# Kernel optimization log

Measured on AMD Instinct MI355X. Metric: run time of the kernel, lower is better.

The kernel has to match this reference:

```python
import jax, jax.numpy as jnp
import numpy as np

B, S, D, E, L = 8, 512, 768, 768, 4000

def setup_inputs() -> dict:
    key = jax.random.key(0)
    k1, k2, k3, k4 = jax.random.split(key, 4)
    last_hidden_state = jax.random.normal(k1, (B, S, D), dtype=jnp.float32)
    label_feat = jax.random.normal(k2, (L, E), dtype=jnp.float32)
    # nn.Linear(D, E): weight [E, D], bias [E]; xavier-ish scale
    W = jax.random.normal(k3, (E, D), dtype=jnp.float32) * (1.0 / np.sqrt(D))
    bias = jax.random.normal(k4, (E,), dtype=jnp.float32) * 0.01
    return {"last_hidden_state": last_hidden_state, "label_feat": label_feat, "W": W, "bias": bias}

def reference(last_hidden_state, label_feat, W, bias):
    # proj: tanh(Linear(last_hidden_state))  -> [B, S, E]
    proj = jnp.tanh(jnp.einsum('bsd,ed->bse', last_hidden_state, W) + bias)
    # scores: bmm(label_feat [B,L,E], proj^T [B,E,S]) -> [B, L, S]
    scores = jnp.einsum('le,bse->bls', label_feat, proj)
    # softmax over dim=1 (the LABEL dim), as in the original
    weights = jax.nn.softmax(scores, axis=1)
    # attn: bmm(weights [B,L,S], last_hidden_state [B,S,D]) -> [B, L, D]
    attn_output = jnp.einsum('bls,bsd->bld', weights, last_hidden_state)
    return (weights, attn_output)
```

## Files before the change

### kernel.cpp

```cpp
#include <hip/hip_runtime.h>
#include <hip/hip_bf16.h>
#include <cmath>

typedef __attribute__((ext_vector_type(8))) short short8;
typedef __attribute__((ext_vector_type(4))) float f32x4;

#define SM_CH 16
#define WCH   32

__device__ inline ushort f2bf(float x) {
    union { float f; unsigned u; } v; v.f = x;
    unsigned r = v.u + 0x7FFF + ((v.u >> 16) & 1);
    return (ushort)(r >> 16);
}

__device__ inline void split2(float x, ushort& hi, ushort& lo) {
    union { float f; unsigned u; } v; v.f = x;
    hi = (ushort)(v.u >> 16);
    union { float f; unsigned u; } h; h.u = v.u & 0xFFFF0000u;
    union { float f; unsigned u; } d; d.f = x - h.f;
    lo = (ushort)(d.u >> 16);
}

__device__ inline int swz(int row, int byte_in_row) {
    return row * 128 + (byte_in_row ^ ((row & 7) << 4));
}

__device__ inline void gload16(const void* g, void* lds) {
    __builtin_amdgcn_global_load_lds(
        (const __attribute__((address_space(1))) unsigned int*)g,
        (__attribute__((address_space(3))) unsigned int*)lds, 16, 0, 0);
}

__device__ inline void xcd_remap(int& bx, int& by, int& bz) {
    unsigned nx = gridDim.x, ny = gridDim.y;
    unsigned nwg = nx * ny * gridDim.z;
    unsigned id = blockIdx.x + nx * (blockIdx.y + ny * blockIdx.z);
    unsigned q = nwg >> 3;
    unsigned s = (id & 7) * q + (id >> 3);
    bx = s % nx; unsigned r = s / nx;
    by = r % ny; bz = r / ny;
}

template<int ROWS, int KS>
__device__ inline void stage_plane(const ushort* __restrict__ src,
                                   char* plane, int t, int rbase, int rmax)
{
    #pragma unroll
    for (int s = 0; s < ROWS / 64; ++s) {
        const int row = s * 64 + (t >> 3);
        const int col = (((t & 7) * 16) ^ ((row & 7) << 4)) >> 1;
        const int gr  = min(rbase + row, rmax);
        gload16(src + (long long)gr * KS + col,
                plane + s * 8192 + (t >> 6) * 1024);
    }
}

template<bool SPLIT3, int BM, int MREP, bool STATS, int NT, int KS, int VMN>
__global__ __launch_bounds__(512, 2) void mfma8(
    const ushort* __restrict__ AH, const ushort* __restrict__ AL,
    const ushort* __restrict__ BH, const ushort* __restrict__ BL,
    float* __restrict__ Cb, float* __restrict__ pmo, float* __restrict__ pso,
    int M, int N, long long sA, long long sB, long long sC)
{
    extern __shared__ char smem[];
    constexpr int ABYTES = BM * 128;

    int bx, by, bz; xcd_remap(bx, by, bz);
    const int bm = bx * BM;
    const int bn = by * 256;
    const long long z = bz;

    const ushort* AHb = AH + z * sA;
    const ushort* ALb = SPLIT3 ? (AL + z * sA) : AHb;
    const ushort* BHb = BH + z * sB;
    const ushort* BLb = SPLIT3 ? (BL + z * sB) : BHb;

    const int t    = threadIdx.x;
    const int lane = t & 63;
    const int w    = t >> 6;
    const int wr   = w >> 2;
    const int wc   = w & 3;
    const int lrow = lane & 15;
    const int kg16 = (lane >> 4) * 16;

    const ushort* Ap; const ushort* Bp; int kc;
#define SELPLANES(tt_)                                                        \
    do {                                                                      \
        if constexpr (SPLIT3) {                                               \
            Ap = ((tt_) < 24) ? AHb : ALb;                                    \
            Bp = (((tt_) < 12) || ((tt_) >= 24)) ? BHb : BLb;                 \
            int seg_ = ((tt_) < 12) ? (tt_) : (((tt_) < 24) ? (tt_) - 12      \
                                                            : (tt_) - 24);   \
            kc = seg_ * 64;                                                   \
        } else { Ap = AHb; Bp = BHb; kc = (tt_) * 64; }                       \
    } while (0)

    SELPLANES(0);
    stage_plane<BM, KS>(Ap + kc, smem, t, bm, M - 1);
    stage_plane<256, KS>(Bp + kc, smem + 2 * ABYTES, t, bn, N - 1);
    SELPLANES(1);
    stage_plane<BM, KS>(Ap + kc, smem + ABYTES, t, bm, M - 1);
    stage_plane<256, KS>(Bp + kc, smem + 2 * ABYTES + 32768, t, bn, N - 1);
    if constexpr (VMN == 8) asm volatile("s_waitcnt vmcnt(8)" ::: "memory");
    else                    asm volatile("s_waitcnt vmcnt(6)" ::: "memory");
    __builtin_amdgcn_s_barrier();

    f32x4 acc[MREP][4] = {};

    for (int tt = 0; tt < NT; ++tt) {
        const int cur = tt & 1;
        char* Ab = smem + cur * ABYTES;
        char* Bb = smem + 2 * ABYTES + cur * 32768;

        __builtin_amdgcn_s_setprio(1);
        short8 bf[4][2];
        #pragma unroll
        for (int n = 0; n < 4; ++n)
            #pragma unroll
            for (int ks = 0; ks < 2; ++ks)
                bf[n][ks] = *(const short8*)(Bb + swz(wc * 64 + n * 16 + lrow,
                                                      ks * 64 + kg16));
        #pragma unroll
        for (int q = 0; q < MREP / 2; ++q) {
            short8 af[2][2];
            #pragma unroll
            for (int mi = 0; mi < 2; ++mi)
                #pragma unroll
                for (int ks = 0; ks < 2; ++ks)
                    af[mi][ks] = *(const short8*)(Ab +
                        swz(wr * (BM / 2) + (q * 2 + mi) * 16 + lrow,
                            ks * 64 + kg16));
            #pragma unroll
            for (int ks = 0; ks < 2; ++ks)
                #pragma unroll
                for (int mi = 0; mi < 2; ++mi)
                    #pragma unroll
                    for (int n = 0; n < 4; ++n)
                        acc[q * 2 + mi][n] = __builtin_amdgcn_mfma_f32_16x16x32_bf16(
                            af[mi][ks], bf[n][ks], acc[q * 2 + mi][n], 0, 0, 0);
        }
        __builtin_amdgcn_s_setprio(0);

        asm volatile("s_waitcnt lgkmcnt(0)" ::: "memory");
        __builtin_amdgcn_s_barrier();

        if (tt + 2 < NT) {
            SELPLANES(tt + 2);
            stage_plane<BM, KS>(Ap + kc, smem + cur * ABYTES, t, bm, M - 1);
            stage_plane<256, KS>(Bp + kc, smem + 2 * ABYTES + cur * 32768,
                                 t, bn, N - 1);
            if constexpr (VMN == 8)
                asm volatile("s_waitcnt vmcnt(8)" ::: "memory");
            else
                asm volatile("s_waitcnt vmcnt(6)" ::: "memory");
        } else {
            asm volatile("s_waitcnt vmcnt(0)" ::: "memory");
        }
        __builtin_amdgcn_s_barrier();
    }
#undef SELPLANES

    float* C = Cb + z * sC;
    const int r0 = bm + wr * (BM / 2) + (lane >> 4) * 4;
    const int c0 = bn + wc * 64 + (lane & 15);
    #pragma unroll
    for (int n = 0; n < 4; ++n) {
        const int col = c0 + n * 16;
        #pragma unroll
        for (int mi = 0; mi < MREP; ++mi) {
            #pragma unroll
            for (int r = 0; r < 4; ++r) {
                const int row = r0 + mi * 16 + r;
                if (row < M) C[(long long)row * N + col] = acc[mi][n][r];
            }
        }
    }

    if constexpr (STATS) {
        __syncthreads();
        float* red = (float*)smem;
        const int slot = wr * 4 + (lane >> 4);
        const int colb = wc * 64 + (lane & 15);

        float lm[4];
        #pragma unroll
        for (int n = 0; n < 4; ++n) {
            float v = -INFINITY;
            #pragma unroll
            for (int mi = 0; mi < MREP; ++mi)
                #pragma unroll
                for (int r = 0; r < 4; ++r)
                    if (r0 + mi * 16 + r < M) v = fmaxf(v, acc[mi][n][r]);
            lm[n] = v;
        }
        #pragma unroll
        for (int n = 0; n < 4; ++n)
            red[(colb + n * 16) * 8 + slot] = lm[n];
        __syncthreads();
        float cm[4];
        #pragma unroll
        for (int n = 0; n < 4; ++n) {
            float v = -INFINITY;
            #pragma unroll
            for (int s8 = 0; s8 < 8; ++s8)
                v = fmaxf(v, red[(colb + n * 16) * 8 + s8]);
            cm[n] = v;
        }
        __syncthreads();
        float ls[4];
        #pragma unroll
        for (int n = 0; n < 4; ++n) {
            float sum = 0.f;
            #pragma unroll
            for (int mi = 0; mi < MREP; ++mi)
                #pragma unroll
                for (int r = 0; r < 4; ++r)
                    if (r0 + mi * 16 + r < M) sum += __expf(acc[mi][n][r] - cm[n]);
            ls[n] = sum;
        }
        #pragma unroll
        for (int n = 0; n < 4; ++n)
            red[(colb + n * 16) * 8 + slot] = ls[n];
        __syncthreads();
        if (slot == 0) {
            #pragma unroll
            for (int n = 0; n < 4; ++n) {
                float sum = 0.f;
                #pragma unroll
                for (int s8 = 0; s8 < 8; ++s8)
                    sum += red[(colb + n * 16) * 8 + s8];
                const int col = bn + colb + n * 16;
                pmo[(z * SM_CH + bx) * N + col] = cm[n];
                pso[(z * SM_CH + bx) * N + col] = sum;
            }
        }
    }
}

__global__ __launch_bounds__(256) void split_planes_kernel(
    const float* __restrict__ in, ushort* __restrict__ H,
    ushort* __restrict__ L, long long n4)
{
    long long i = (long long)blockIdx.x * 256 + threadIdx.x;
    if (i >= n4) return;
    float4 v = *(const float4*)(in + i * 4);
    ushort h[4], l[4];
    split2(v.x, h[0], l[0]); split2(v.y, h[1], l[1]);
    split2(v.z, h[2], l[2]); split2(v.w, h[3], l[3]);
    *(ushort4*)(H + i * 4) = *(ushort4*)h;
    *(ushort4*)(L + i * 4) = *(ushort4*)l;
}

__global__ __launch_bounds__(256) void mfma_proj(
    const float* __restrict__ Ab, const float* __restrict__ Bb,
    ushort* __restrict__ CH, ushort* __restrict__ CL,
    const float* __restrict__ bias, int M, int N, int K)
{
    extern __shared__ char smem[];
    char* Ah = smem;
    char* Al = smem + 16384;
    char* Bh = smem + 32768;
    char* Bl = smem + 49152;

    int bx, by, bz; xcd_remap(bx, by, bz);
    const int bm = bx * 128;
    const int bn = by * 128;

    const int t  = threadIdx.x;
    const int srow = t >> 1;
    const int skh  = (t & 1) * 32;
    const float* ap = Ab + (long long)min(bm + srow, M - 1) * K + skh;
    const float* bp = Bb + (long long)min(bn + srow, N - 1) * K + skh;

    const int lane = t & 63;
    const int w    = t >> 6;
    const int wm   = (w >> 1) * 64;
    const int wn   = (w & 1) * 64;
    const int lrow = lane & 15;
    const int kg16 = (lane >> 4) * 16;

    f32x4 acc[4][4] = {};

    for (int k0 = 0; k0 < K; k0 += 64) {
        #pragma unroll
        for (int j = 0; j < 4; ++j) {
            float xs[8];
            *(float4*)&xs[0] = *(const float4*)(ap + k0 + j * 8);
            *(float4*)&xs[4] = *(const float4*)(ap + k0 + j * 8 + 4);
            ushort oh[8], ol[8];
            #pragma unroll
            for (int i = 0; i < 8; ++i) split2(xs[i], oh[i], ol[i]);
            const int off = swz(srow, skh * 2 + j * 16);
            *(uint4*)(Ah + off) = *(uint4*)oh;
            *(uint4*)(Al + off) = *(uint4*)ol;
        }
        #pragma unroll
        for (int j = 0; j < 4; ++j) {
            float xs[8];
            *(float4*)&xs[0] = *(const float4*)(bp + k0 + j * 8);
            *(float4*)&xs[4] = *(const float4*)(bp + k0 + j * 8 + 4);
            ushort oh[8], ol[8];
            #pragma unroll
            for (int i = 0; i < 8; ++i) split2(xs[i], oh[i], ol[i]);
            const int off = swz(srow, skh * 2 + j * 16);
            *(uint4*)(Bh + off) = *(uint4*)oh;
            *(uint4*)(Bl + off) = *(uint4*)ol;
        }
        __syncthreads();

        #pragma unroll
        for (int kk = 0; kk < 2; ++kk) {
            short8 ah[4], al[4];
            #pragma unroll
            for (int mi = 0; mi < 4; ++mi) {
                const int off = swz(wm + mi * 16 + lrow, kk * 64 + kg16);
                ah[mi] = *(const short8*)(Ah + off);
                al[mi] = *(const short8*)(Al + off);
            }
            #pragma unroll
            for (int ni = 0; ni < 4; ++ni) {
                const int off = swz(wn + ni * 16 + lrow, kk * 64 + kg16);
                short8 bh = *(const short8*)(Bh + off);
                short8 bl = *(const short8*)(Bl + off);
                #pragma unroll
                for (int mi = 0; mi < 4; ++mi) {
                    acc[mi][ni] = __builtin_amdgcn_mfma_f32_16x16x32_bf16(al[mi], bh, acc[mi][ni], 0, 0, 0);
                    acc[mi][ni] = __builtin_amdgcn_mfma_f32_16x16x32_bf16(ah[mi], bl, acc[mi][ni], 0, 0, 0);
                    acc[mi][ni] = __builtin_amdgcn_mfma_f32_16x16x32_bf16(ah[mi], bh, acc[mi][ni], 0, 0, 0);
                }
            }
        }
        __syncthreads();
    }

    const int r0 = bm + wm + (lane >> 4) * 4;
    const int c0 = bn + wn + (lane & 15);
    #pragma unroll
    for (int ni = 0; ni < 4; ++ni) {
        const int col = c0 + ni * 16;
        const float bv = bias[col];
        #pragma unroll
        for (int mi = 0; mi < 4; ++mi) {
            #pragma unroll
            for (int r = 0; r < 4; ++r) {
                const int row = r0 + mi * 16 + r;
                if (row < M) {
                    float x = tanhf(acc[mi][ni][r] + bv);
                    ushort h, l;
                    split2(x, h, l);
                    CH[(long long)row * N + col] = h;
                    CL[(long long)row * N + col] = l;
                }
            }
        }
    }
}

__global__ __launch_bounds__(256) void transpose_bf16_kernel(
    const float* __restrict__ in, ushort* __restrict__ out, int S, int D)
{
    __shared__ float tile[32][33];
    const int b = blockIdx.z;
    const int s0 = blockIdx.x * 32, d0 = blockIdx.y * 32;
    const int tx = threadIdx.x & 31, ty = threadIdx.x >> 5;
    const float* ip = in + (long long)b * S * D;
    #pragma unroll
    for (int i = 0; i < 32; i += 8)
        tile[ty + i][tx] = ip[(long long)(s0 + ty + i) * D + d0 + tx];
    __syncthreads();
    ushort* op = out + (long long)b * S * D;
    #pragma unroll
    for (int i = 0; i < 32; i += 8)
        op[(long long)(d0 + ty + i) * S + s0 + tx] = f2bf(tile[tx][ty + i]);
}

__global__ __launch_bounds__(256) void softmax_merge_kernel(
    const float* __restrict__ pm, const float* __restrict__ ps,
    float* __restrict__ fm, float* __restrict__ fsinv, int S)
{
    int s = blockIdx.x * 256 + threadIdx.x;
    int b = blockIdx.y;
    float m = -INFINITY;
    #pragma unroll
    for (int c = 0; c < SM_CH; ++c)
        m = fmaxf(m, pm[(b * SM_CH + c) * S + s]);
    float sum = 0.f;
    #pragma unroll
    for (int c = 0; c < SM_CH; ++c)
        sum += ps[(b * SM_CH + c) * S + s] * __expf(pm[(b * SM_CH + c) * S + s] - m);
    fm[b * S + s] = m;
    fsinv[b * S + s] = 1.f / sum;
}

__global__ __launch_bounds__(256) void softmax_write_kernel(
    float* __restrict__ scores, const float* __restrict__ fm,
    const float* __restrict__ fsinv, int L, int S, int chlen,
    ushort* __restrict__ wbf)
{
    int s = blockIdx.x * 256 + threadIdx.x;
    int c = blockIdx.y;
    int b = blockIdx.z;
    float m   = fm[b * S + s];
    float inv = fsinv[b * S + s];
    float* p = scores + (long long)b * L * S + s;
    ushort* q = wbf + (long long)b * L * S + s;
    int l0 = c * chlen;
    int l1 = min(L, l0 + chlen);
    for (int l = l0; l < l1; ++l) {
        float x = p[(long long)l * S];
        float v = __expf(x - m) * inv;
        p[(long long)l * S] = v;
        q[(long long)l * S] = f2bf(v);
    }
}

extern "C" void kernel_launch(void* const* d_in, const int* in_sizes, int n_in,
                              void* d_out, int out_size, void* d_ws, size_t ws_size,
                              hipStream_t stream)
{
    const int Bn = 8, S = 512, D = 768, E = 768, L = 4000;
    const float* lhs   = (const float*)d_in[0];
    const float* label = (const float*)d_in[1];
    const float* W     = (const float*)d_in[2];
    const float* bias  = (const float*)d_in[3];

    float* weights = (float*)d_out;
    float* attn    = (float*)d_out + (long long)Bn * L * S;

    const long long nLE  = (long long)L * E;
    const long long nBSE = (long long)Bn * S * E;
    const long long nBDS = (long long)Bn * D * S;
    const long long nBLS = (long long)Bn * L * S;

    ushort* labelH = (ushort*)d_ws;
    ushort* labelL = labelH + nLE;
    ushort* projH  = labelL + nLE;
    ushort* projL  = projH + nBSE;
    ushort* lhsT   = projL + nBSE;
    ushort* wbf    = lhsT + nBDS;
    float*  pm     = (float*)(wbf + nBLS);
    float*  ps     = pm + Bn * SM_CH * S;
    float*  fm     = ps + Bn * SM_CH * S;
    float*  fsinv  = fm + Bn * S;

    auto scoresK = mfma8<true, 256, 8, true, 36, 768, 8>;
    auto attnK   = mfma8<false, 128, 4, false, 8, 512, 6>;
    hipFuncSetAttribute((const void*)scoresK,
                        hipFuncAttributeMaxDynamicSharedMemorySize, 131072);
    hipFuncSetAttribute((const void*)attnK,
                        hipFuncAttributeMaxDynamicSharedMemorySize, 98304);

    transpose_bf16_kernel<<<dim3(S / 32, D / 32, Bn), 256, 0, stream>>>(
        lhs, lhsT, S, D);
    split_planes_kernel<<<(int)(nLE / 4 + 255) / 256, 256, 0, stream>>>(
        label, labelH, labelL, nLE / 4);

    mfma_proj<<<dim3((Bn * S) / 128, E / 128, 1), 256, 65536, stream>>>(
        lhs, W, projH, projL, bias, Bn * S, E, D);

    scoresK<<<dim3((L + 255) / 256, S / 256, Bn), 512, 131072, stream>>>(
        labelH, labelL, projH, projL, weights, pm, ps,
        L, S, 0LL, (long long)S * E, (long long)L * S);

    softmax_merge_kernel<<<dim3(S / 256, Bn), 256, 0, stream>>>(
        pm, ps, fm, fsinv, S);
    softmax_write_kernel<<<dim3(S / 256, WCH, Bn), 256, 0, stream>>>(
        weights, fm, fsinv, L, S, (L + WCH - 1) / WCH, wbf);

    attnK<<<dim3((L + 127) / 128, D / 256, Bn), 512, 98304, stream>>>(
        wbf, nullptr, lhsT, nullptr, attn, nullptr, nullptr,
        L, D, (long long)L * S, (long long)D * S, (long long)L * D);
}
```

Measured before the change: 250.8 us.

## Stage hi/lo bf16 planes together in scores GEMM and fold softmax merge into write

The split-bf16 scores GEMM now loads the hi and lo halves of each 32-wide K chunk into one LDS tile and issues all three cross products (lo·hi, hi·lo, hi·hi) from one set of fragment reads. This replaces three separate 12-step K passes over different plane pairs with 24 steps. The aim is to read each A and B plane once instead of re-reading the hi planes, and to raise MFMA density per LDS load. Separately, the softmax merge kernel is removed and its max/sum reduction is recomputed in every softmax-write block. That saves one launch but repeats the small merge work across the 32 chunks.

New measurement: 243.9 us, median of 3. 2.7% less time.

```diff
diff --git a/kernel.cpp b/kernel.cpp
--- a/kernel.cpp
+++ b/kernel.cpp
@@ -42,39 +42,22 @@
     by = r % ny; bz = r / ny;
 }
 
-template<int ROWS, int KS>
-__device__ inline void stage_plane(const ushort* __restrict__ src,
-                                   char* plane, int t, int rbase, int rmax)
-{
-    #pragma unroll
-    for (int s = 0; s < ROWS / 64; ++s) {
-        const int row = s * 64 + (t >> 3);
-        const int col = (((t & 7) * 16) ^ ((row & 7) << 4)) >> 1;
-        const int gr  = min(rbase + row, rmax);
-        gload16(src + (long long)gr * KS + col,
-                plane + s * 8192 + (t >> 6) * 1024);
-    }
-}
-
-template<bool SPLIT3, int BM, int MREP, bool STATS, int NT, int KS, int VMN>
-__global__ __launch_bounds__(512, 2) void mfma8(
+__global__ __launch_bounds__(512, 2) void mfma_sc2(
     const ushort* __restrict__ AH, const ushort* __restrict__ AL,
     const ushort* __restrict__ BH, const ushort* __restrict__ BL,
     float* __restrict__ Cb, float* __restrict__ pmo, float* __restrict__ pso,
-    int M, int N, long long sA, long long sB, long long sC)
+    int M, int N, long long sB, long long sC)
 {
     extern __shared__ char smem[];
-    constexpr int ABYTES = BM * 128;
+    const int K = 768;
 
     int bx, by, bz; xcd_remap(bx, by, bz);
-    const int bm = bx * BM;
+    const int bm = bx * 256;
     const int bn = by * 256;
     const long long z = bz;
 
-    const ushort* AHb = AH + z * sA;
-    const ushort* ALb = SPLIT3 ? (AL + z * sA) : AHb;
     const ushort* BHb = BH + z * sB;
-    const ushort* BLb = SPLIT3 ? (BL + z * sB) : BHb;
+    const ushort* BLb = BL + z * sB;
 
     const int t    = threadIdx.x;
     const int lane = t & 63;
@@ -84,29 +67,203 @@
     const int lrow = lane & 15;
     const int kg16 = (lane >> 4) * 16;
 
-    const ushort* Ap; const ushort* Bp; int kc;
-#define SELPLANES(tt_)                                                        \
-    do {                                                                      \
-        if constexpr (SPLIT3) {                                               \
-            Ap = ((tt_) < 24) ? AHb : ALb;                                    \
-            Bp = (((tt_) < 12) || ((tt_) >= 24)) ? BHb : BLb;                 \
-            int seg_ = ((tt_) < 12) ? (tt_) : (((tt_) < 24) ? (tt_) - 12      \
-                                                            : (tt_) - 24);   \
-            kc = seg_ * 64;                                                   \
-        } else { Ap = AHb; Bp = BHb; kc = (tt_) * 64; }                       \
-    } while (0)
-
-    SELPLANES(0);
-    stage_plane<BM, KS>(Ap + kc, smem, t, bm, M - 1);
-    stage_plane<256, KS>(Bp + kc, smem + 2 * ABYTES, t, bn, N - 1);
-    SELPLANES(1);
-    stage_plane<BM, KS>(Ap + kc, smem + ABYTES, t, bm, M - 1);
-    stage_plane<256, KS>(Bp + kc, smem + 2 * ABYTES + 32768, t, bn, N - 1);
-    if constexpr (VMN == 8) asm volatile("s_waitcnt vmcnt(8)" ::: "memory");
-    else                    asm volatile("s_waitcnt vmcnt(6)" ::: "memory");
+    const ushort* srcA[4]; const ushort* srcB[4]; int ldsO[4];
+    #pragma unroll
+    for (int i = 0; i < 4; ++i) {
+        const int row  = w * 32 + i * 8 + (lane >> 3);
+        const int q    = (lane & 7) ^ (row & 7);
+        const int colo = (q & 3) * 8;
+        srcA[i] = ((q < 4) ? AH : AL) + (long long)min(bm + row, M - 1) * K + colo;
+        srcB[i] = ((q < 4) ? BHb : BLb) + (long long)(bn + row) * K + colo;
+        ldsO[i] = w * 4096 + i * 1024;
+    }
+
+#define STAGE(k0_, cur_)                                                      \
+    {                                                                         \
+        _Pragma("unroll")                                                     \
+        for (int i = 0; i < 4; ++i) {                                         \
+            gload16(srcA[i] + (k0_), smem + (cur_) * 32768 + ldsO[i]);        \
+            gload16(srcB[i] + (k0_), smem + 65536 + (cur_) * 32768 + ldsO[i]);\
+        }                                                                     \
+    }
+
+    STAGE(0, 0);
+    STAGE(32, 1);
+    asm volatile("s_waitcnt vmcnt(8)" ::: "memory");
     __builtin_amdgcn_s_barrier();
 
-    f32x4 acc[MREP][4] = {};
+    f32x4 acc[8][4] = {};
+
+    for (int tt = 0; tt < 24; ++tt) {
+        const int cur = tt & 1;
+        const char* Ab = smem + cur * 32768;
+        const char* Bb = smem + 65536 + cur * 32768;
+
+        __builtin_amdgcn_s_setprio(1);
+        short8 bh[4], bl[4];
+        #pragma unroll
+        for (int n = 0; n < 4; ++n) {
+            bh[n] = *(const short8*)(Bb + swz(wc * 64 + n * 16 + lrow, kg16));
+            bl[n] = *(const short8*)(Bb + swz(wc * 64 + n * 16 + lrow, 64 + kg16));
+        }
+        #pragma unroll
+        for (int g = 0; g < 2; ++g) {
+            short8 ah[4], al[4];
+            #pragma unroll
+            for (int m4 = 0; m4 < 4; ++m4) {
+                const int r = wr * 128 + (g * 4 + m4) * 16 + lrow;
+                ah[m4] = *(const short8*)(Ab + swz(r, kg16));
+                al[m4] = *(const short8*)(Ab + swz(r, 64 + kg16));
+            }
+            #pragma unroll
+            for (int m4 = 0; m4 < 4; ++m4)
+                #pragma unroll
+                for (int n = 0; n < 4; ++n) {
+                    acc[g*4+m4][n] = __builtin_amdgcn_mfma_f32_16x16x32_bf16(
+                        al[m4], bh[n], acc[g*4+m4][n], 0, 0, 0);
+                    acc[g*4+m4][n] = __builtin_amdgcn_mfma_f32_16x16x32_bf16(
+                        ah[m4], bl[n], acc[g*4+m4][n], 0, 0, 0);
+                    acc[g*4+m4][n] = __builtin_amdgcn_mfma_f32_16x16x32_bf16(
+                        ah[m4], bh[n], acc[g*4+m4][n], 0, 0, 0);
+                }
+        }
+        __builtin_amdgcn_s_setprio(0);
+
+        asm volatile("s_waitcnt lgkmcnt(0)" ::: "memory");
+        __builtin_amdgcn_s_barrier();
+
+        if (tt + 2 < 24) {
+            STAGE((tt + 2) * 32, cur);
+            asm volatile("s_waitcnt vmcnt(8)" ::: "memory");
+        } else {
+            asm volatile("s_waitcnt vmcnt(0)" ::: "memory");
+        }
+        __builtin_amdgcn_s_barrier();
+    }
+#undef STAGE
+
+    float* C = Cb + z * sC;
+    const int r0 = bm + wr * 128 + (lane >> 4) * 4;
+    const int c0 = bn + wc * 64 + (lane & 15);
+    #pragma unroll
+    for (int n = 0; n < 4; ++n) {
+        const int col = c0 + n * 16;
+        #pragma unroll
+        for (int mi = 0; mi < 8; ++mi) {
+            #pragma unroll
+            for (int r = 0; r < 4; ++r) {
+                const int row = r0 + mi * 16 + r;
+                if (row < M) C[(long long)row * N + col] = acc[mi][n][r];
+            }
+        }
+    }
+
+    __syncthreads();
+    float* red = (float*)smem;
+    const int slot = wr * 4 + (lane >> 4);
+    const int colb = wc * 64 + (lane & 15);
+
+    float lm[4];
+    #pragma unroll
+    for (int n = 0; n < 4; ++n) {
+        float v = -INFINITY;
+        #pragma unroll
+        for (int mi = 0; mi < 8; ++mi)
+            #pragma unroll
+            for (int r = 0; r < 4; ++r)
+                if (r0 + mi * 16 + r < M) v = fmaxf(v, acc[mi][n][r]);
+        lm[n] = v;
+    }
+    #pragma unroll
+    for (int n = 0; n < 4; ++n)
+        red[(colb + n * 16) * 8 + slot] = lm[n];
+    __syncthreads();
+    float cm[4];
+    #pragma unroll
+    for (int n = 0; n < 4; ++n) {
+        float v = -INFINITY;
+        #pragma unroll
+        for (int s8 = 0; s8 < 8; ++s8)
+            v = fmaxf(v, red[(colb + n * 16) * 8 + s8]);
+        cm[n] = v;
+    }
+    __syncthreads();
+    float ls[4];
+    #pragma unroll
+    for (int n = 0; n < 4; ++n) {
+        float sum = 0.f;
+        #pragma unroll
+        for (int mi = 0; mi < 8; ++mi)
+            #pragma unroll
+            for (int r = 0; r < 4; ++r)
+                if (r0 + mi * 16 + r < M) sum += __expf(acc[mi][n][r] - cm[n]);
+        ls[n] = sum;
+    }
+    #pragma unroll
+    for (int n = 0; n < 4; ++n)
+        red[(colb + n * 16) * 8 + slot] = ls[n];
+    __syncthreads();
+    if (slot == 0) {
+        #pragma unroll
+        for (int n = 0; n < 4; ++n) {
+            float sum = 0.f;
+            #pragma unroll
+            for (int s8 = 0; s8 < 8; ++s8)
+                sum += red[(colb + n * 16) * 8 + s8];
+            const int col = bn + colb + n * 16;
+            pmo[(z * SM_CH + bx) * N + col] = cm[n];
+            pso[(z * SM_CH + bx) * N + col] = sum;
+        }
+    }
+}
+
+template<int ROWS, int KS>
+__device__ inline void stage_plane(const ushort* __restrict__ src,
+                                   char* plane, int t, int rbase, int rmax)
+{
+    #pragma unroll
+    for (int s = 0; s < ROWS / 64; ++s) {
+        const int row = s * 64 + (t >> 3);
+        const int col = (((t & 7) * 16) ^ ((row & 7) << 4)) >> 1;
+        const int gr  = min(rbase + row, rmax);
+        gload16(src + (long long)gr * KS + col,
+                plane + s * 8192 + (t >> 6) * 1024);
+    }
+}
+
+__global__ __launch_bounds__(512, 2) void mfma_attn8(
+    const ushort* __restrict__ A, const ushort* __restrict__ B,
+    float* __restrict__ Cb, int M, int N,
+    long long sA, long long sB, long long sC)
+{
+    extern __shared__ char smem[];
+    constexpr int ABYTES = 128 * 128;
+    constexpr int NT = 8, KS = 512;
+
+    int bx, by, bz; xcd_remap(bx, by, bz);
+    const int bm = bx * 128;
+    const int bn = by * 256;
+    const long long z = bz;
+
+    const ushort* Ab_g = A + z * sA;
+    const ushort* Bb_g = B + z * sB;
+
+    const int t    = threadIdx.x;
+    const int lane = t & 63;
+    const int w    = t >> 6;
+    const int wr   = w >> 2;
+    const int wc   = w & 3;
+    const int lrow = lane & 15;
+    const int kg16 = (lane >> 4) * 16;
+
+    stage_plane<128, KS>(Ab_g, smem, t, bm, M - 1);
+    stage_plane<256, KS>(Bb_g, smem + 2 * ABYTES, t, bn, N - 1);
+    stage_plane<128, KS>(Ab_g + 64, smem + ABYTES, t, bm, M - 1);
+    stage_plane<256, KS>(Bb_g + 64, smem + 2 * ABYTES + 32768, t, bn, N - 1);
+    asm volatile("s_waitcnt vmcnt(6)" ::: "memory");
+    __builtin_amdgcn_s_barrier();
+
+    f32x4 acc[4][4] = {};
 
     for (int tt = 0; tt < NT; ++tt) {
         const int cur = tt & 1;
@@ -122,15 +279,14 @@
                 bf[n][ks] = *(const short8*)(Bb + swz(wc * 64 + n * 16 + lrow,
                                                       ks * 64 + kg16));
         #pragma unroll
-        for (int q = 0; q < MREP / 2; ++q) {
+        for (int q = 0; q < 2; ++q) {
             short8 af[2][2];
             #pragma unroll
             for (int mi = 0; mi < 2; ++mi)
                 #pragma unroll
                 for (int ks = 0; ks < 2; ++ks)
                     af[mi][ks] = *(const short8*)(Ab +
-                        swz(wr * (BM / 2) + (q * 2 + mi) * 16 + lrow,
-                            ks * 64 + kg16));
+                        swz(wr * 64 + (q * 2 + mi) * 16 + lrow, ks * 64 + kg16));
             #pragma unroll
             for (int ks = 0; ks < 2; ++ks)
                 #pragma unroll
@@ -146,93 +302,29 @@
         __builtin_amdgcn_s_barrier();
 
         if (tt + 2 < NT) {
-            SELPLANES(tt + 2);
-            stage_plane<BM, KS>(Ap + kc, smem + cur * ABYTES, t, bm, M - 1);
-            stage_plane<256, KS>(Bp + kc, smem + 2 * ABYTES + cur * 32768,
-                                 t, bn, N - 1);
-            if constexpr (VMN == 8)
-                asm volatile("s_waitcnt vmcnt(8)" ::: "memory");
-            else
-                asm volatile("s_waitcnt vmcnt(6)" ::: "memory");
+            stage_plane<128, KS>(Ab_g + (tt + 2) * 64, smem + cur * ABYTES,
+                                 t, bm, M - 1);
+            stage_plane<256, KS>(Bb_g + (tt + 2) * 64,
+                                 smem + 2 * ABYTES + cur * 32768, t, bn, N - 1);
+            asm volatile("s_waitcnt vmcnt(6)" ::: "memory");
         } else {
             asm volatile("s_waitcnt vmcnt(0)" ::: "memory");
         }
         __builtin_amdgcn_s_barrier();
     }
-#undef SELPLANES
 
     float* C = Cb + z * sC;
-    const int r0 = bm + wr * (BM / 2) + (lane >> 4) * 4;
+    const int r0 = bm + wr * 64 + (lane >> 4) * 4;
     const int c0 = bn + wc * 64 + (lane & 15);
     #pragma unroll
     for (int n = 0; n < 4; ++n) {
         const int col = c0 + n * 16;
         #pragma unroll
-        for (int mi = 0; mi < MREP; ++mi) {
+        for (int mi = 0; mi < 4; ++mi) {
             #pragma unroll
             for (int r = 0; r < 4; ++r) {
                 const int row = r0 + mi * 16 + r;
                 if (row < M) C[(long long)row * N + col] = acc[mi][n][r];
-            }
-        }
-    }
-
-    if constexpr (STATS) {
-        __syncthreads();
-        float* red = (float*)smem;
-        const int slot = wr * 4 + (lane >> 4);
-        const int colb = wc * 64 + (lane & 15);
-
-        float lm[4];
-        #pragma unroll
-        for (int n = 0; n < 4; ++n) {
-            float v = -INFINITY;
-            #pragma unroll
-            for (int mi = 0; mi < MREP; ++mi)
-                #pragma unroll
-                for (int r = 0; r < 4; ++r)
-                    if (r0 + mi * 16 + r < M) v = fmaxf(v, acc[mi][n][r]);
-            lm[n] = v;
-        }
-        #pragma unroll
-        for (int n = 0; n < 4; ++n)
-            red[(colb + n * 16) * 8 + slot] = lm[n];
-        __syncthreads();
-        float cm[4];
-        #pragma unroll
-        for (int n = 0; n < 4; ++n) {
-            float v = -INFINITY;
-            #pragma unroll
-            for (int s8 = 0; s8 < 8; ++s8)
-                v = fmaxf(v, red[(colb + n * 16) * 8 + s8]);
-            cm[n] = v;
-        }
-        __syncthreads();
-        float ls[4];
-        #pragma unroll
-        for (int n = 0; n < 4; ++n) {
-            float sum = 0.f;
-            #pragma unroll
-            for (int mi = 0; mi < MREP; ++mi)
-                #pragma unroll
-                for (int r = 0; r < 4; ++r)
-                    if (r0 + mi * 16 + r < M) sum += __expf(acc[mi][n][r] - cm[n]);
-            ls[n] = sum;
-        }
-        #pragma unroll
-        for (int n = 0; n < 4; ++n)
-            red[(colb + n * 16) * 8 + slot] = ls[n];
-        __syncthreads();
-        if (slot == 0) {
-            #pragma unroll
-            for (int n = 0; n < 4; ++n) {
-                float sum = 0.f;
-                #pragma unroll
-                for (int s8 = 0; s8 < 8; ++s8)
-                    sum += red[(colb + n * 16) * 8 + s8];
-                const int col = bn + colb + n * 16;
-                pmo[(z * SM_CH + bx) * N + col] = cm[n];
-                pso[(z * SM_CH + bx) * N + col] = sum;
             }
         }
     }
@@ -375,34 +467,25 @@
         op[(long long)(d0 + ty + i) * S + s0 + tx] = f2bf(tile[tx][ty + i]);
 }
 
-__global__ __launch_bounds__(256) void softmax_merge_kernel(
-    const float* __restrict__ pm, const float* __restrict__ ps,
-    float* __restrict__ fm, float* __restrict__ fsinv, int S)
-{
-    int s = blockIdx.x * 256 + threadIdx.x;
-    int b = blockIdx.y;
-    float m = -INFINITY;
-    #pragma unroll
-    for (int c = 0; c < SM_CH; ++c)
-        m = fmaxf(m, pm[(b * SM_CH + c) * S + s]);
-    float sum = 0.f;
-    #pragma unroll
-    for (int c = 0; c < SM_CH; ++c)
-        sum += ps[(b * SM_CH + c) * S + s] * __expf(pm[(b * SM_CH + c) * S + s] - m);
-    fm[b * S + s] = m;
-    fsinv[b * S + s] = 1.f / sum;
-}
-
-__global__ __launch_bounds__(256) void softmax_write_kernel(
-    float* __restrict__ scores, const float* __restrict__ fm,
-    const float* __restrict__ fsinv, int L, int S, int chlen,
+__global__ __launch_bounds__(256) void softmax_write2_kernel(
+    float* __restrict__ scores, const float* __restrict__ pm,
+    const float* __restrict__ ps, int L, int S, int chlen,
     ushort* __restrict__ wbf)
 {
     int s = blockIdx.x * 256 + threadIdx.x;
     int c = blockIdx.y;
     int b = blockIdx.z;
-    float m   = fm[b * S + s];
-    float inv = fsinv[b * S + s];
+
+    float m = -INFINITY;
+    #pragma unroll
+    for (int k = 0; k < SM_CH; ++k)
+        m = fmaxf(m, pm[(b * SM_CH + k) * S + s]);
+    float sum = 0.f;
+    #pragma unroll
+    for (int k = 0; k < SM_CH; ++k)
+        sum += ps[(b * SM_CH + k) * S + s] * __expf(pm[(b * SM_CH + k) * S + s] - m);
+    float inv = 1.f / sum;
+
     float* p = scores + (long long)b * L * S + s;
     ushort* q = wbf + (long long)b * L * S + s;
     int l0 = c * chlen;
@@ -441,14 +524,10 @@
     ushort* wbf    = lhsT + nBDS;
     float*  pm     = (float*)(wbf + nBLS);
     float*  ps     = pm + Bn * SM_CH * S;
-    float*  fm     = ps + Bn * SM_CH * S;
-    float*  fsinv  = fm + Bn * S;
-
-    auto scoresK = mfma8<true, 256, 8, true, 36, 768, 8>;
-    auto attnK   = mfma8<false, 128, 4, false, 8, 512, 6>;
-    hipFuncSetAttribute((const void*)scoresK,
+
+    hipFuncSetAttribute((const void*)mfma_sc2,
                         hipFuncAttributeMaxDynamicSharedMemorySize, 131072);
-    hipFuncSetAttribute((const void*)attnK,
+    hipFuncSetAttribute((const void*)mfma_attn8,
                         hipFuncAttributeMaxDynamicSharedMemorySize, 98304);
 
     transpose_bf16_kernel<<<dim3(S / 32, D / 32, Bn), 256, 0, stream>>>(
@@ -459,16 +538,14 @@
     mfma_proj<<<dim3((Bn * S) / 128, E / 128, 1), 256, 65536, stream>>>(
         lhs, W, projH, projL, bias, Bn * S, E, D);
 
-    scoresK<<<dim3((L + 255) / 256, S / 256, Bn), 512, 131072, stream>>>(
+    mfma_sc2<<<dim3((L + 255) / 256, S / 256, Bn), 512, 131072, stream>>>(
         labelH, labelL, projH, projL, weights, pm, ps,
-        L, S, 0LL, (long long)S * E, (long long)L * S);
-
-    softmax_merge_kernel<<<dim3(S / 256, Bn), 256, 0, stream>>>(
-        pm, ps, fm, fsinv, S);
-    softmax_write_kernel<<<dim3(S / 256, WCH, Bn), 256, 0, stream>>>(
-        weights, fm, fsinv, L, S, (L + WCH - 1) / WCH, wbf);
-
-    attnK<<<dim3((L + 127) / 128, D / 256, Bn), 512, 98304, stream>>>(
-        wbf, nullptr, lhsT, nullptr, attn, nullptr, nullptr,
-        L, D, (long long)L * S, (long long)D * S, (long long)L * D);
-}
+        L, S, (long long)S * E, (long long)L * S);
+
+    softmax_write2_kernel<<<dim3(S / 256, WCH, Bn), 256, 0, stream>>>(
+        weights, pm, ps, L, S, (L + WCH - 1) / WCH, wbf);
+
+    mfma_attn8<<<dim3((L + 127) / 128, D / 256, Bn), 512, 98304, stream>>>(
+        wbf, lhsT, attn, L, D,
+        (long long)L * S, (long long)D * S, (long long)L * D);
+}
```
